# Kernel optimization log

Hardware: AMD Instinct MI355X
Metric: run time of the kernel (lower is better)

## Reference

```python
import jax, jax.numpy as jnp
import numpy as np

D_MODEL = 1024
HIDDEN = 2048
D_STATE = 16
KERN = 3
BATCH = 2
SEQ = 2048


def _layernorm(x, g, b, eps=1e-5):
    m = jnp.mean(x, axis=-1, keepdims=True)
    v = jnp.var(x, axis=-1, keepdims=True)
    return (x - m) * jax.lax.rsqrt(v + eps) * g + b


def setup_inputs() -> dict:
    key = jax.random.key(0)
    ks = jax.random.split(key, 10)
    w_scale = 0.02  # keep pre-activations in a sane range (mimics trained-net init)
    return {
        "x": jax.random.normal(ks[0], (BATCH, SEQ, D_MODEL), jnp.float32),
        "W_x": jax.random.normal(ks[1], (HIDDEN, D_MODEL), jnp.float32) * w_scale,
        "b_x": jnp.zeros((HIDDEN,), jnp.float32),
        "W_g": jax.random.normal(ks[2], (HIDDEN, D_MODEL), jnp.float32) * w_scale,
        "b_g": jnp.zeros((HIDDEN,), jnp.float32),
        "conv_w": jax.random.normal(ks[3], (HIDDEN, 1, KERN), jnp.float32) * 0.3,
        "conv_b": jnp.zeros((HIDDEN,), jnp.float32),
        "A_raw": jax.random.normal(ks[4], (HIDDEN, D_STATE), jnp.float32),
        "B_ssm": jax.random.normal(ks[5], (HIDDEN, D_STATE), jnp.float32),
        "C_ssm": jax.random.normal(ks[6], (HIDDEN, D_STATE), jnp.float32),
        "W_dt": jax.random.normal(ks[7], (HIDDEN, D_MODEL), jnp.float32) * w_scale,
        "b_dt": jnp.zeros((HIDDEN,), jnp.float32),
        "W_out": jax.random.normal(ks[8], (D_MODEL, HIDDEN), jnp.float32) * w_scale,
        "b_out": jnp.zeros((D_MODEL,), jnp.float32),
        "ln_g": jnp.ones((D_MODEL,), jnp.float32),
        "ln_b": jnp.zeros((D_MODEL,), jnp.float32),
    }


def reference(x, W_x, b_x, W_g, b_g, conv_w, conv_b, A_raw, B_ssm, C_ssm,
              W_dt, b_dt, W_out, b_out, ln_g, ln_b):
    # projections: u, gate
    u = jnp.einsum('bld,hd->blh', x, W_x) + b_x                    # [B,L,H]
    g = jax.nn.sigmoid(jnp.einsum('bld,hd->blh', x, W_g) + b_g)    # [B,L,H]
    # depthwise conv over time (padding = kernel//2, 'same' for odd kernel)
    pad = conv_w.shape[-1] // 2
    h = jax.lax.conv_general_dilated(
        jnp.transpose(u, (0, 2, 1)), conv_w,
        window_strides=(1,), padding=[(pad, pad)],
        feature_group_count=conv_w.shape[0],
        dimension_numbers=('NCH', 'OIH', 'NCH')) + conv_b[None, :, None]
    h = jnp.transpose(h, (0, 2, 1))                                # [B,L,H]
    u = u * g + h * (1.0 - g)
    # time-invariant dt per channel (mean over batch & time, clamped)
    dt = jax.nn.softplus(jnp.einsum('bld,hd->blh', x, W_dt) + b_dt).mean(axis=(0, 1))
    dt = jnp.clip(dt, 1e-3, 2.0)                                   # [H]
    # discretize
    A = -jax.nn.softplus(A_raw)                                    # [H,S]
    A_d = jnp.exp(A * dt[:, None])                                 # [H,S]
    B_d = (A_d - 1.0) / (A + 1e-6) * B_ssm                         # [H,S]
    # selective scan: state s[b,h,k] = A_d*s + B_d*u_t ; y = <s, C>
    Bsz, L, H = u.shape
    S = A_d.shape[1]

    def step(carry, u_t):                                          # u_t: [B,H]
        new = A_d[None] * carry + B_d[None] * u_t[:, :, None]      # [B,H,S]
        y_t = jnp.einsum('bhs,hs->bh', new, C_ssm)
        return new, y_t

    init = jnp.zeros((Bsz, H, S), dtype=u.dtype)
    _, ys = jax.lax.scan(step, init, jnp.transpose(u, (1, 0, 2)))  # ys: [L,B,H]
    y = jnp.transpose(ys, (1, 0, 2))                               # [B,L,H]
    out = jnp.einsum('blh,dh->bld', y, W_out) + b_out
    return _layernorm(x + out, ln_g, ln_b)
```

## Files before the change

### kernel.cpp

```cpp
#include <hip/hip_runtime.h>
#include <math.h>

#define D_MODEL 1024
#define HIDDEN  2048
#define D_STATE 16
#define BATCH   2
#define SEQ     2048
#define NTOK    (BATCH*SEQ)
#define CHUNK   32
#define NCHUNK  (SEQ/CHUNK)

typedef __attribute__((ext_vector_type(8))) short bf16x8;
typedef __attribute__((ext_vector_type(8))) unsigned short ushort8;
typedef __attribute__((ext_vector_type(4))) float f32x4;

#define GLOAD_LDS16(gptr, lptr) \
    __builtin_amdgcn_global_load_lds((const __attribute__((address_space(1))) void*)(gptr), \
                                     (__attribute__((address_space(3))) void*)(lptr), 16, 0, 0)

__device__ __forceinline__ float softplus_f(float x) {
    return fmaxf(x, 0.0f) + log1pf(expf(-fabsf(x)));
}
__device__ __forceinline__ float sigmoid_f(float x) {
    return 1.0f / (1.0f + expf(-x));
}
__device__ __forceinline__ ushort f2bf(float f) {
    unsigned u = __float_as_uint(f);
    unsigned r = (u + 0x7fffu + ((u >> 16) & 1u)) >> 16;
    return (ushort)r;
}
__device__ __forceinline__ float bf2f(ushort u) {
    return __uint_as_float(((unsigned)u) << 16);
}

__global__ __launch_bounds__(256) void cvt_all(
    const float* __restrict__ x, const float* __restrict__ Wx,
    const float* __restrict__ Wg, const float* __restrict__ Wdt,
    const float* __restrict__ Wout, ushort* __restrict__ arena)
{
    int i = blockIdx.x * 256 + threadIdx.x;
    const float* src; int base;
    if      (i < 1048576) { src = x;    base = 0; }
    else if (i < 1572864) { src = Wx;   base = 1048576; }
    else if (i < 2097152) { src = Wg;   base = 1572864; }
    else if (i < 2621440) { src = Wdt;  base = 2097152; }
    else                  { src = Wout; base = 2621440; }
    float4 v = reinterpret_cast<const float4*>(src)[i - base];
    ushort4 o = { f2bf(v.x), f2bf(v.y), f2bf(v.z), f2bf(v.w) };
    reinterpret_cast<ushort4*>(arena)[i] = o;
}

__global__ __launch_bounds__(256) void proj_gemm_fused(
    const ushort* __restrict__ xbf, const ushort* __restrict__ Wcat,
    const float* __restrict__ b_x, const float* __restrict__ b_g,
    const float* __restrict__ b_dt, ushort* __restrict__ u_out,
    ushort* __restrict__ g_out, float* __restrict__ dt_sum)
{
    __shared__ ushort S[16384];
    ushort* As = S;
    ushort* Bs = S + 4096;
    const int tid = threadIdx.x, lane = tid & 63, w = tid >> 6;
    const int wm = w & 1, wn = w >> 1;
    const int m0 = blockIdx.x * 128, n0 = blockIdx.y * 128;
    const int quad = lane >> 4, fr = lane & 15;
    const int lr   = lane >> 2;
    const int qsrc = (lane & 3) ^ ((lane >> 3) & 3);
    const int chq  = quad ^ ((fr >> 1) & 3);
    const int K = D_MODEL;

    const size_t ga0 = (size_t)(m0 + w * 16 + lr) * K + qsrc * 8;
    const size_t ga1 = ga0 + (size_t)64 * K;
    const size_t gb0 = (size_t)(n0 + w * 16 + lr) * K + qsrc * 8;
    const size_t gb1 = gb0 + (size_t)64 * K;

    f32x4 acc[4][4];
    #pragma unroll
    for (int i = 0; i < 4; i++)
        #pragma unroll
        for (int j = 0; j < 4; j++)
            acc[i][j] = (f32x4){0.f, 0.f, 0.f, 0.f};

    for (int t = 0; t < K / 32; t++) {
        const size_t koff = (size_t)t * 32;
        GLOAD_LDS16(xbf  + ga0 + koff, &As[w * 512]);
        GLOAD_LDS16(xbf  + ga1 + koff, &As[2048 + w * 512]);
        GLOAD_LDS16(Wcat + gb0 + koff, &Bs[w * 512]);
        GLOAD_LDS16(Wcat + gb1 + koff, &Bs[2048 + w * 512]);
        asm volatile("s_waitcnt vmcnt(0) lgkmcnt(0)" ::: "memory");
        asm volatile("s_barrier" ::: "memory");

        bf16x8 af[4], bfv[4];
        #pragma unroll
        for (int q = 0; q < 4; q++) {
            af[q]  = *reinterpret_cast<const bf16x8*>(&As[(wm * 64 + q * 16 + fr) * 32 + chq * 8]);
            bfv[q] = *reinterpret_cast<const bf16x8*>(&Bs[(wn * 64 + q * 16 + fr) * 32 + chq * 8]);
        }
        #pragma unroll
        for (int ii = 0; ii < 4; ii++)
            #pragma unroll
            for (int jj = 0; jj < 4; jj++)
                acc[ii][jj] = __builtin_amdgcn_mfma_f32_16x16x32_bf16(af[ii], bfv[jj], acc[ii][jj], 0, 0, 0);
        asm volatile("s_barrier" ::: "memory");
    }

    const int region = n0 >> 11;
    const int ncb = n0 & 2047;

    if (region == 2) {
        #pragma unroll
        for (int j = 0; j < 4; j++) {
            int n = ncb + wn * 64 + j * 16 + fr;
            float bj = b_dt[n];
            float s = 0.f;
            #pragma unroll
            for (int i = 0; i < 4; i++)
                #pragma unroll
                for (int r = 0; r < 4; r++)
                    s += softplus_f(acc[i][j][r] + bj);
            s += __shfl_xor(s, 16);
            s += __shfl_xor(s, 32);
            if (lane < 16) atomicAdd(&dt_sum[n], s);
        }
    } else {
        const float* bias = region ? b_g : b_x;
        ushort* out = region ? g_out : u_out;
        ushort* Cs = S;
        __syncthreads();
        #pragma unroll
        for (int j = 0; j < 4; j++) {
            int col = wn * 64 + j * 16 + fr;
            float bj = bias[ncb + col];
            #pragma unroll
            for (int i = 0; i < 4; i++) {
                int row = wm * 64 + i * 16 + quad * 4;
                #pragma unroll
                for (int r = 0; r < 4; r++) {
                    float v = acc[i][j][r] + bj;
                    if (region) v = sigmoid_f(v);
                    Cs[(row + r) * 128 + col] = f2bf(v);
                }
            }
        }
        __syncthreads();
        #pragma unroll
        for (int k = 0; k < 8; k++) {
            int v = k * 256 + tid;
            int row = v >> 4, c = (v & 15) * 8;
            *reinterpret_cast<ushort8*>(&out[(size_t)(m0 + row) * HIDDEN + ncb + c]) =
                *reinterpret_cast<const ushort8*>(&Cs[v * 8]);
        }
    }
}

__global__ __launch_bounds__(256) void gemm_out64(
    const ushort* __restrict__ ybf, const ushort* __restrict__ Wout,
    const float* __restrict__ b_out, const float* __restrict__ x,
    float* __restrict__ resid)
{
    __shared__ ushort S[36864];
    ushort* As = S;
    ushort* Bs = S + 12288;
    const int tid = threadIdx.x, lane = tid & 63, w = tid >> 6;
    const int m0 = blockIdx.x * 64, n0 = blockIdx.y * 128;
    const int quad = lane >> 4, fr = lane & 15;
    const int lr8  = lane >> 3;
    const int q8   = (lane & 7) ^ (lr8 & 7);
    const int K = HIDDEN;

    const size_t ga = (size_t)(m0 + w * 16 + lr8) * K + q8 * 8;
    const size_t gb = (size_t)(n0 + w * 32 + lr8) * K + q8 * 8;

    f32x4 acc[4][2];
    #pragma unroll
    for (int i = 0; i < 4; i++)
        #pragma unroll
        for (int j = 0; j < 2; j++)
            acc[i][j] = (f32x4){0.f, 0.f, 0.f, 0.f};

#define STAGE_OUT(KT, BUF) do {                                                   \
    const size_t ko_ = (size_t)(KT) * 64;                                         \
    GLOAD_LDS16(ybf  + ga + ko_,            &As[(BUF)*4096 + (w*2+0)*512]);       \
    GLOAD_LDS16(ybf  + ga + 8*K + ko_,      &As[(BUF)*4096 + (w*2+1)*512]);       \
    GLOAD_LDS16(Wout + gb + ko_,            &Bs[(BUF)*8192 + (w*4+0)*512]);       \
    GLOAD_LDS16(Wout + gb + 8*K + ko_,      &Bs[(BUF)*8192 + (w*4+1)*512]);       \
    GLOAD_LDS16(Wout + gb + 16*K + ko_,     &Bs[(BUF)*8192 + (w*4+2)*512]);       \
    GLOAD_LDS16(Wout + gb + 24*K + ko_,     &Bs[(BUF)*8192 + (w*4+3)*512]);       \
  } while (0)

    STAGE_OUT(0, 0);
    STAGE_OUT(1, 1);

    int buf = 0;
    for (int t = 0; t < 32; t++) {
        asm volatile("s_waitcnt vmcnt(6) lgkmcnt(0)" ::: "memory");
        asm volatile("s_barrier" ::: "memory");
        int nb = buf + 2; if (nb >= 3) nb -= 3;
        const int kt = (t + 2 < 32) ? (t + 2) : 0;
        STAGE_OUT(kt, nb);

        const ushort* as = &As[buf * 4096];
        const ushort* bs = &Bs[buf * 8192];
        #pragma unroll
        for (int ks = 0; ks < 2; ks++) {
            const int ch = ((ks * 4 + quad) ^ (fr & 7)) * 8;
            bf16x8 af[4], bfv[2];
            #pragma unroll
            for (int mi = 0; mi < 4; mi++)
                af[mi] = *reinterpret_cast<const bf16x8*>(&as[(mi * 16 + fr) * 64 + ch]);
            #pragma unroll
            for (int nj = 0; nj < 2; nj++)
                bfv[nj] = *reinterpret_cast<const bf16x8*>(&bs[(w * 32 + nj * 16 + fr) * 64 + ch]);
            #pragma unroll
            for (int mi = 0; mi < 4; mi++)
                #pragma unroll
                for (int nj = 0; nj < 2; nj++)
                    acc[mi][nj] = __builtin_amdgcn_mfma_f32_16x16x32_bf16(af[mi], bfv[nj], acc[mi][nj], 0, 0, 0);
        }
        buf = (buf == 2) ? 0 : buf + 1;
    }
    asm volatile("s_waitcnt vmcnt(0) lgkmcnt(0)" ::: "memory");
    asm volatile("s_barrier" ::: "memory");
#undef STAGE_OUT

    float* Sf = (float*)S;
    #pragma unroll
    for (int nj = 0; nj < 2; nj++) {
        int col = w * 32 + nj * 16 + fr;
        float bj = b_out[n0 + col];
        #pragma unroll
        for (int mi = 0; mi < 4; mi++) {
            int row = mi * 16 + quad * 4;
            #pragma unroll
            for (int r = 0; r < 4; r++)
                Sf[(row + r) * 128 + col] = acc[mi][nj][r] + bj;
        }
    }
    __syncthreads();
    #pragma unroll
    for (int k = 0; k < 8; k++) {
        int v = k * 256 + tid;
        int row = v >> 5, c = (v & 31) * 4;
        size_t off = (size_t)(m0 + row) * D_MODEL + n0 + c;
        float4 xa = *reinterpret_cast<const float4*>(&x[off]);
        float4 cv = *reinterpret_cast<const float4*>(&Sf[v * 4]);
        float4 o = { cv.x + xa.x, cv.y + xa.y, cv.z + xa.z, cv.w + xa.w };
        *reinterpret_cast<float4*>(&resid[off]) = o;
    }
}

__global__ __launch_bounds__(256) void dt_finalize(
    const float* __restrict__ dt_sum, const float* __restrict__ A_raw,
    const float* __restrict__ B_ssm, float* __restrict__ A_d,
    float* __restrict__ B_d, float* __restrict__ A_dL)
{
    int i = blockIdx.x * 256 + threadIdx.x;
    if (i >= HIDDEN * D_STATE) return;
    int h = i >> 4;
    float dt = dt_sum[h] * (1.0f / NTOK);
    dt = fminf(fmaxf(dt, 1e-3f), 2.0f);
    float Av = -softplus_f(A_raw[i]);
    float Ad = expf(Av * dt);
    float Bd = (Ad - 1.0f) / (Av + 1e-6f) * B_ssm[i];
    A_d[i] = Ad;
    B_d[i] = Bd;
    A_dL[i] = expf(Av * dt * CHUNK);
}

__global__ __launch_bounds__(256) void scan_pass1(
    const ushort* __restrict__ u_bf, const ushort* __restrict__ g_bf,
    const float* __restrict__ conv_w, const float* __restrict__ conv_b,
    const float* __restrict__ A_d, const float* __restrict__ B_d,
    const float* __restrict__ C_ssm,
    ushort* __restrict__ ypart, float* __restrict__ states)
{
    int idx = blockIdx.x * 256 + threadIdx.x;
    int h  = idx & (HIDDEN - 1);
    int bc = idx >> 11;
    int c  = bc & (NCHUNK - 1);
    int b  = bc / NCHUNK;
    float Ad[D_STATE], Bd[D_STATE], Cv[D_STATE], st[D_STATE];
    const float4* a4 = reinterpret_cast<const float4*>(A_d  + h * D_STATE);
    const float4* b4 = reinterpret_cast<const float4*>(B_d  + h * D_STATE);
    const float4* c4 = reinterpret_cast<const float4*>(C_ssm + h * D_STATE);
    #pragma unroll
    for (int q = 0; q < 4; q++) {
        float4 av = a4[q], bv = b4[q], cv = c4[q];
        Ad[q*4+0]=av.x; Ad[q*4+1]=av.y; Ad[q*4+2]=av.z; Ad[q*4+3]=av.w;
        Bd[q*4+0]=bv.x; Bd[q*4+1]=bv.y; Bd[q*4+2]=bv.z; Bd[q*4+3]=bv.w;
        Cv[q*4+0]=cv.x; Cv[q*4+1]=cv.y; Cv[q*4+2]=cv.z; Cv[q*4+3]=cv.w;
    }
    #pragma unroll
    for (int s = 0; s < D_STATE; s++) st[s] = 0.f;

    float w0 = conv_w[h * 3 + 0], w1 = conv_w[h * 3 + 1];
    float w2 = conv_w[h * 3 + 2], cb = conv_b[h];
    const int tok0 = c * CHUNK;
    const size_t base = ((size_t)b * SEQ + tok0) * HIDDEN + h;
    float u_prev = (tok0 > 0) ? bf2f(u_bf[base - HIDDEN]) : 0.f;
    float u_cur  = bf2f(u_bf[base]);
    for (int l = 0; l < CHUNK; l++) {
        float u_next = (tok0 + l + 1 < SEQ) ? bf2f(u_bf[base + (size_t)(l + 1) * HIDDEN]) : 0.f;
        float gv = bf2f(g_bf[base + (size_t)l * HIDDEN]);
        float conv = u_prev * w0 + u_cur * w1 + u_next * w2 + cb;
        float uv = u_cur * gv + conv * (1.0f - gv);
        float y0 = 0.f, y1 = 0.f, y2 = 0.f, y3 = 0.f;
        #pragma unroll
        for (int s = 0; s < D_STATE; s += 4) {
            st[s+0] = fmaf(Ad[s+0], st[s+0], Bd[s+0] * uv);
            st[s+1] = fmaf(Ad[s+1], st[s+1], Bd[s+1] * uv);
            st[s+2] = fmaf(Ad[s+2], st[s+2], Bd[s+2] * uv);
            st[s+3] = fmaf(Ad[s+3], st[s+3], Bd[s+3] * uv);
            y0 = fmaf(st[s+0], Cv[s+0], y0);
            y1 = fmaf(st[s+1], Cv[s+1], y1);
            y2 = fmaf(st[s+2], Cv[s+2], y2);
            y3 = fmaf(st[s+3], Cv[s+3], y3);
        }
        ypart[base + (size_t)l * HIDDEN] = f2bf((y0 + y1) + (y2 + y3));
        u_prev = u_cur; u_cur = u_next;
    }
    float4* sp = reinterpret_cast<float4*>(states + ((size_t)bc * HIDDEN + h) * D_STATE);
    #pragma unroll
    for (int q = 0; q < 4; q++)
        sp[q] = (float4){st[q*4+0], st[q*4+1], st[q*4+2], st[q*4+3]};
}

__global__ __launch_bounds__(256) void scan_pass2(
    float* __restrict__ states, const float* __restrict__ A_dL)
{
    int idx = blockIdx.x * 256 + threadIdx.x;
    int s = idx & 15;
    int h = (idx >> 4) & (HIDDEN - 1);
    int b = idx >> 15;
    float aL = A_dL[h * D_STATE + s];
    float carry = 0.f;
    const size_t cstride = (size_t)HIDDEN * D_STATE;
    float* p = states + ((size_t)b * NCHUNK * HIDDEN + h) * D_STATE + s;
    #pragma unroll 1
    for (int cb = 0; cb < NCHUNK / 8; cb++) {
        float fin[8];
        #pragma unroll
        for (int j = 0; j < 8; j++) fin[j] = p[(size_t)j * cstride];
        #pragma unroll
        for (int j = 0; j < 8; j++) {
            p[(size_t)j * cstride] = carry;
            carry = fmaf(aL, carry, fin[j]);
        }
        p += 8 * cstride;
    }
}

__global__ __launch_bounds__(256) void scan_pass3(
    const ushort* __restrict__ ypart, const float* __restrict__ states,
    const float* __restrict__ A_d, const float* __restrict__ C_ssm,
    ushort* __restrict__ ybf)
{
    int idx = blockIdx.x * 256 + threadIdx.x;
    int h  = idx & (HIDDEN - 1);
    int bc = idx >> 11;
    int c  = bc & (NCHUNK - 1);
    int b  = bc / NCHUNK;
    float Ad[D_STATE], t[D_STATE];
    const float* sp = states + ((size_t)bc * HIDDEN + h) * D_STATE;
    #pragma unroll
    for (int s = 0; s < D_STATE; s++) {
        float a = A_d[h * D_STATE + s];
        Ad[s] = a;
        t[s] = C_ssm[h * D_STATE + s] * a * sp[s];
    }
    const size_t base = ((size_t)b * SEQ + (size_t)c * CHUNK) * HIDDEN + h;
    for (int l = 0; l < CHUNK; l++) {
        float c0 = 0.f, c1 = 0.f;
        #pragma unroll
        for (int s = 0; s < D_STATE; s += 2) {
            c0 += t[s];
            c1 += t[s + 1];
            t[s] *= Ad[s];
            t[s + 1] *= Ad[s + 1];
        }
        ybf[base + (size_t)l * HIDDEN] = f2bf(bf2f(ypart[base + (size_t)l * HIDDEN]) + (c0 + c1));
    }
}

__global__ __launch_bounds__(256) void ln_kernel(
    const float* __restrict__ resid, const float* __restrict__ ln_g,
    const float* __restrict__ ln_b, float* __restrict__ out)
{
    int row = blockIdx.x;
    int tid = threadIdx.x;
    const float4 v = reinterpret_cast<const float4*>(resid + (size_t)row * D_MODEL)[tid];
    float s  = v.x + v.y + v.z + v.w;
    float ss = v.x * v.x + v.y * v.y + v.z * v.z + v.w * v.w;
    #pragma unroll
    for (int off = 32; off > 0; off >>= 1) {
        s  += __shfl_down(s, off);
        ss += __shfl_down(ss, off);
    }
    __shared__ float sbuf[4], ssbuf[4];
    int wid = tid >> 6, lane = tid & 63;
    if (lane == 0) { sbuf[wid] = s; ssbuf[wid] = ss; }
    __syncthreads();
    float tot  = sbuf[0] + sbuf[1] + sbuf[2] + sbuf[3];
    float tot2 = ssbuf[0] + ssbuf[1] + ssbuf[2] + ssbuf[3];
    float mean = tot * (1.0f / D_MODEL);
    float var  = tot2 * (1.0f / D_MODEL) - mean * mean;
    float rstd = rsqrtf(var + 1e-5f);
    const float4 gv = reinterpret_cast<const float4*>(ln_g)[tid];
    const float4 bv = reinterpret_cast<const float4*>(ln_b)[tid];
    float4 o;
    o.x = (v.x - mean) * rstd * gv.x + bv.x;
    o.y = (v.y - mean) * rstd * gv.y + bv.y;
    o.z = (v.z - mean) * rstd * gv.z + bv.z;
    o.w = (v.w - mean) * rstd * gv.w + bv.w;
    reinterpret_cast<float4*>(out + (size_t)row * D_MODEL)[tid] = o;
}

extern "C" void kernel_launch(void* const* d_in, const int* in_sizes, int n_in,
                              void* d_out, int out_size, void* d_ws, size_t ws_size,
                              hipStream_t stream) {
    const float* x      = (const float*)d_in[0];
    const float* W_x    = (const float*)d_in[1];
    const float* b_x    = (const float*)d_in[2];
    const float* W_g    = (const float*)d_in[3];
    const float* b_g    = (const float*)d_in[4];
    const float* conv_w = (const float*)d_in[5];
    const float* conv_b = (const float*)d_in[6];
    const float* A_raw  = (const float*)d_in[7];
    const float* B_ssm  = (const float*)d_in[8];
    const float* C_ssm  = (const float*)d_in[9];
    const float* W_dt   = (const float*)d_in[10];
    const float* b_dt   = (const float*)d_in[11];
    const float* W_out  = (const float*)d_in[12];
    const float* b_out  = (const float*)d_in[13];
    const float* ln_g   = (const float*)d_in[14];
    const float* ln_b   = (const float*)d_in[15];

    char* W = (char*)d_ws;
    ushort* arena   = (ushort*)(W);
    ushort* x_bf    = arena;
    ushort* Wcat    = arena + 4194304;
    ushort* Wout_bf = arena + 10485760;
    ushort* u_bf    = (ushort*)(W + (24ull << 20));
    ushort* g_bf    = (ushort*)(W + (40ull << 20));
    ushort* ypart   = (ushort*)(W + (56ull << 20));
    float*  resid   = (float*)(W + (40ull << 20));
    float*  states  = (float*)(W);
    float*  dt_sum  = (float*)(W + (80ull << 20));
    float*  A_d     = (float*)(W + (80ull << 20) + 65536);
    float*  B_d     = (float*)(W + (80ull << 20) + 65536 + 131072);
    float*  A_dL    = (float*)(W + (80ull << 20) + 65536 + 262144);
    ushort* y_bf    = u_bf;

    hipMemsetAsync(dt_sum, 0, HIDDEN * sizeof(float), stream);

    dim3 blk(256);
    cvt_all<<<12288, blk, 0, stream>>>(x, W_x, W_g, W_dt, W_out, arena);

    dim3 grid_proj(NTOK / 128, 3 * HIDDEN / 128);
    proj_gemm_fused<<<grid_proj, blk, 0, stream>>>(x_bf, Wcat, b_x, b_g, b_dt,
                                                   u_bf, g_bf, dt_sum);
    dt_finalize<<<(HIDDEN * D_STATE) / 256, blk, 0, stream>>>(dt_sum, A_raw, B_ssm,
                                                              A_d, B_d, A_dL);
    scan_pass1<<<(BATCH * NCHUNK * HIDDEN) / 256, blk, 0, stream>>>(
        u_bf, g_bf, conv_w, conv_b, A_d, B_d, C_ssm, ypart, states);
    scan_pass2<<<(BATCH * HIDDEN * D_STATE) / 256, blk, 0, stream>>>(states, A_dL);
    scan_pass3<<<(BATCH * NCHUNK * HIDDEN) / 256, blk, 0, stream>>>(ypart, states, A_d,
                                                                    C_ssm, y_bf);
    dim3 grid_out(NTOK / 64, D_MODEL / 128);
    gemm_out64<<<grid_out, blk, 0, stream>>>(y_bf, Wout_bf, b_out, x, resid);
    ln_kernel<<<NTOK, blk, 0, stream>>>(resid, ln_g, ln_b, (float*)d_out);
}
```

Measured before the change: 306.3 us.

## Enlarge projection GEMM tile to 256x128 with triple-buffered async LDS pipeline

The projection GEMM moves from a 128x128 tile, where each wave computes 64x64, to a 256x128 tile where each wave computes 64x128 (4x8 MFMA accumulators). The global-to-LDS loads now use a three-buffer ring, prefetching two k-steps ahead and waiting with a partial vmcnt, so memory latency overlaps with MFMA work instead of stalling on every step. The aim is more data reuse per LDS load and better latency hiding. In exchange it uses more registers and LDS per block, and halves the grid along M, which may lower occupancy.

Result: no change. 303.3 us (-1.0%).

```diff
diff --git a/kernel.cpp b/kernel.cpp
--- a/kernel.cpp
+++ b/kernel.cpp
@@ -50,73 +50,88 @@
     reinterpret_cast<ushort4*>(arena)[i] = o;
 }
 
-__global__ __launch_bounds__(256) void proj_gemm_fused(
+__global__ __launch_bounds__(256, 2) void proj_gemm_fused(
     const ushort* __restrict__ xbf, const ushort* __restrict__ Wcat,
     const float* __restrict__ b_x, const float* __restrict__ b_g,
     const float* __restrict__ b_dt, ushort* __restrict__ u_out,
     ushort* __restrict__ g_out, float* __restrict__ dt_sum)
 {
-    __shared__ ushort S[16384];
+    __shared__ ushort S[36864];
     ushort* As = S;
-    ushort* Bs = S + 4096;
+    ushort* Bs = S + 24576;
     const int tid = threadIdx.x, lane = tid & 63, w = tid >> 6;
-    const int wm = w & 1, wn = w >> 1;
-    const int m0 = blockIdx.x * 128, n0 = blockIdx.y * 128;
+    const int m0 = blockIdx.x * 256, n0 = blockIdx.y * 128;
     const int quad = lane >> 4, fr = lane & 15;
     const int lr   = lane >> 2;
     const int qsrc = (lane & 3) ^ ((lane >> 3) & 3);
     const int chq  = quad ^ ((fr >> 1) & 3);
     const int K = D_MODEL;
 
-    const size_t ga0 = (size_t)(m0 + w * 16 + lr) * K + qsrc * 8;
-    const size_t ga1 = ga0 + (size_t)64 * K;
-    const size_t gb0 = (size_t)(n0 + w * 16 + lr) * K + qsrc * 8;
-    const size_t gb1 = gb0 + (size_t)64 * K;
-
-    f32x4 acc[4][4];
+    const size_t gaB = (size_t)(m0 + w * 64 + lr) * K + qsrc * 8;
+    const size_t gbB = (size_t)(n0 + w * 32 + lr) * K + qsrc * 8;
+
+    f32x4 acc[4][8];
     #pragma unroll
     for (int i = 0; i < 4; i++)
         #pragma unroll
-        for (int j = 0; j < 4; j++)
+        for (int j = 0; j < 8; j++)
             acc[i][j] = (f32x4){0.f, 0.f, 0.f, 0.f};
 
-    for (int t = 0; t < K / 32; t++) {
-        const size_t koff = (size_t)t * 32;
-        GLOAD_LDS16(xbf  + ga0 + koff, &As[w * 512]);
-        GLOAD_LDS16(xbf  + ga1 + koff, &As[2048 + w * 512]);
-        GLOAD_LDS16(Wcat + gb0 + koff, &Bs[w * 512]);
-        GLOAD_LDS16(Wcat + gb1 + koff, &Bs[2048 + w * 512]);
-        asm volatile("s_waitcnt vmcnt(0) lgkmcnt(0)" ::: "memory");
+#define STAGE_P(KT, BUF) do {                                                     \
+    const size_t ko_ = (size_t)(KT) * 32;                                         \
+    GLOAD_LDS16(xbf  + gaB + 0 * 16 * K + ko_, &As[(BUF)*8192 + (w*64 +  0)*32]); \
+    GLOAD_LDS16(xbf  + gaB + 1 * 16 * K + ko_, &As[(BUF)*8192 + (w*64 + 16)*32]); \
+    GLOAD_LDS16(xbf  + gaB + 2 * 16 * K + ko_, &As[(BUF)*8192 + (w*64 + 32)*32]); \
+    GLOAD_LDS16(xbf  + gaB + 3 * 16 * K + ko_, &As[(BUF)*8192 + (w*64 + 48)*32]); \
+    GLOAD_LDS16(Wcat + gbB + 0 * 16 * K + ko_, &Bs[(BUF)*4096 + (w*32 +  0)*32]); \
+    GLOAD_LDS16(Wcat + gbB + 1 * 16 * K + ko_, &Bs[(BUF)*4096 + (w*32 + 16)*32]); \
+  } while (0)
+
+    STAGE_P(0, 0);
+    STAGE_P(1, 1);
+
+    int buf = 0;
+    for (int t = 0; t < 32; t++) {
+        asm volatile("s_waitcnt vmcnt(6) lgkmcnt(0)" ::: "memory");
         asm volatile("s_barrier" ::: "memory");
-
-        bf16x8 af[4], bfv[4];
-        #pragma unroll
-        for (int q = 0; q < 4; q++) {
-            af[q]  = *reinterpret_cast<const bf16x8*>(&As[(wm * 64 + q * 16 + fr) * 32 + chq * 8]);
-            bfv[q] = *reinterpret_cast<const bf16x8*>(&Bs[(wn * 64 + q * 16 + fr) * 32 + chq * 8]);
-        }
-        #pragma unroll
-        for (int ii = 0; ii < 4; ii++)
-            #pragma unroll
-            for (int jj = 0; jj < 4; jj++)
-                acc[ii][jj] = __builtin_amdgcn_mfma_f32_16x16x32_bf16(af[ii], bfv[jj], acc[ii][jj], 0, 0, 0);
-        asm volatile("s_barrier" ::: "memory");
-    }
+        int nb = buf + 2; if (nb >= 3) nb -= 3;
+        const int kt = (t + 2 < 32) ? (t + 2) : 0;
+        STAGE_P(kt, nb);
+
+        const ushort* as = &As[buf * 8192];
+        const ushort* bs = &Bs[buf * 4096];
+        bf16x8 af[4], bfv[8];
+        #pragma unroll
+        for (int mi = 0; mi < 4; mi++)
+            af[mi] = *reinterpret_cast<const bf16x8*>(&as[(w * 64 + mi * 16 + fr) * 32 + chq * 8]);
+        #pragma unroll
+        for (int nj = 0; nj < 8; nj++)
+            bfv[nj] = *reinterpret_cast<const bf16x8*>(&bs[(nj * 16 + fr) * 32 + chq * 8]);
+        #pragma unroll
+        for (int mi = 0; mi < 4; mi++)
+            #pragma unroll
+            for (int nj = 0; nj < 8; nj++)
+                acc[mi][nj] = __builtin_amdgcn_mfma_f32_16x16x32_bf16(af[mi], bfv[nj], acc[mi][nj], 0, 0, 0);
+        buf = (buf == 2) ? 0 : buf + 1;
+    }
+    asm volatile("s_waitcnt vmcnt(0) lgkmcnt(0)" ::: "memory");
+    asm volatile("s_barrier" ::: "memory");
+#undef STAGE_P
 
     const int region = n0 >> 11;
     const int ncb = n0 & 2047;
 
     if (region == 2) {
         #pragma unroll
-        for (int j = 0; j < 4; j++) {
-            int n = ncb + wn * 64 + j * 16 + fr;
+        for (int nj = 0; nj < 8; nj++) {
+            int n = ncb + nj * 16 + fr;
             float bj = b_dt[n];
             float s = 0.f;
             #pragma unroll
-            for (int i = 0; i < 4; i++)
+            for (int mi = 0; mi < 4; mi++)
                 #pragma unroll
                 for (int r = 0; r < 4; r++)
-                    s += softplus_f(acc[i][j][r] + bj);
+                    s += softplus_f(acc[mi][nj][r] + bj);
             s += __shfl_xor(s, 16);
             s += __shfl_xor(s, 32);
             if (lane < 16) atomicAdd(&dt_sum[n], s);
@@ -127,15 +142,15 @@
         ushort* Cs = S;
         __syncthreads();
         #pragma unroll
-        for (int j = 0; j < 4; j++) {
-            int col = wn * 64 + j * 16 + fr;
+        for (int nj = 0; nj < 8; nj++) {
+            int col = nj * 16 + fr;
             float bj = bias[ncb + col];
             #pragma unroll
-            for (int i = 0; i < 4; i++) {
-                int row = wm * 64 + i * 16 + quad * 4;
+            for (int mi = 0; mi < 4; mi++) {
+                int row = w * 64 + mi * 16 + quad * 4;
                 #pragma unroll
                 for (int r = 0; r < 4; r++) {
-                    float v = acc[i][j][r] + bj;
+                    float v = acc[mi][nj][r] + bj;
                     if (region) v = sigmoid_f(v);
                     Cs[(row + r) * 128 + col] = f2bf(v);
                 }
@@ -143,7 +158,7 @@
         }
         __syncthreads();
         #pragma unroll
-        for (int k = 0; k < 8; k++) {
+        for (int k = 0; k < 16; k++) {
             int v = k * 256 + tid;
             int row = v >> 4, c = (v & 15) * 8;
             *reinterpret_cast<ushort8*>(&out[(size_t)(m0 + row) * HIDDEN + ncb + c]) =
@@ -455,7 +470,7 @@
     dim3 blk(256);
     cvt_all<<<12288, blk, 0, stream>>>(x, W_x, W_g, W_dt, W_out, arena);
 
-    dim3 grid_proj(NTOK / 128, 3 * HIDDEN / 128);
+    dim3 grid_proj(NTOK / 256, 3 * HIDDEN / 128);
     proj_gemm_fused<<<grid_proj, blk, 0, stream>>>(x_bf, Wcat, b_x, b_g, b_dt,
                                                    u_bf, g_bf, dt_sum);
     dt_finalize<<<(HIDDEN * D_STATE) / 256, blk, 0, stream>>>(dt_sum, A_raw, B_ssm,
```

## Pipeline projection GEMM with triple-buffered A and register-direct B loads

Applied to the files above, without the earlier changes.

Rewrites the projection GEMM main loop so the activation tile is staged into a three-slot LDS ring two steps ahead, while weight fragments are loaded straight from global memory into registers and double-buffered, with partial vmcnt waits in place of full drains. This is meant to hide global-load latency behind the MFMA work that previously sat idle waiting on each tile. Separately, the dt_sum zeroing memset is folded into the conversion kernel to remove one launch. The trade-offs are more registers in use and uncoalesced per-lane weight reads that skip LDS, which may lower occupancy or bandwidth efficiency.

New measurement: 354.1 us. 15.6% more time.

```diff
diff --git a/kernel.cpp b/kernel.cpp
--- a/kernel.cpp
+++ b/kernel.cpp
@@ -36,8 +36,14 @@
 __global__ __launch_bounds__(256) void cvt_all(
     const float* __restrict__ x, const float* __restrict__ Wx,
     const float* __restrict__ Wg, const float* __restrict__ Wdt,
-    const float* __restrict__ Wout, ushort* __restrict__ arena)
-{
+    const float* __restrict__ Wout, ushort* __restrict__ arena,
+    float* __restrict__ dt_sum)
+{
+    if (blockIdx.x == 0) {
+        float4 z = {0.f, 0.f, 0.f, 0.f};
+        reinterpret_cast<float4*>(dt_sum)[threadIdx.x]       = z;
+        reinterpret_cast<float4*>(dt_sum)[256 + threadIdx.x] = z;
+    }
     int i = blockIdx.x * 256 + threadIdx.x;
     const float* src; int base;
     if      (i < 1048576) { src = x;    base = 0; }
@@ -58,7 +64,6 @@
 {
     __shared__ ushort S[16384];
     ushort* As = S;
-    ushort* Bs = S + 4096;
     const int tid = threadIdx.x, lane = tid & 63, w = tid >> 6;
     const int wm = w & 1, wn = w >> 1;
     const int m0 = blockIdx.x * 128, n0 = blockIdx.y * 128;
@@ -68,10 +73,12 @@
     const int chq  = quad ^ ((fr >> 1) & 3);
     const int K = D_MODEL;
 
-    const size_t ga0 = (size_t)(m0 + w * 16 + lr) * K + qsrc * 8;
-    const size_t ga1 = ga0 + (size_t)64 * K;
-    const size_t gb0 = (size_t)(n0 + w * 16 + lr) * K + qsrc * 8;
-    const size_t gb1 = gb0 + (size_t)64 * K;
+    const size_t ga0 = (size_t)(m0 + w * 32 + lr) * K + qsrc * 8;
+    const size_t ga1 = ga0 + (size_t)16 * K;
+    const size_t gb0 = (size_t)(n0 + wn * 64 +  0 + fr) * K + quad * 8;
+    const size_t gb1 = (size_t)(n0 + wn * 64 + 16 + fr) * K + quad * 8;
+    const size_t gb2 = (size_t)(n0 + wn * 64 + 32 + fr) * K + quad * 8;
+    const size_t gb3 = (size_t)(n0 + wn * 64 + 48 + fr) * K + quad * 8;
 
     f32x4 acc[4][4];
     #pragma unroll
@@ -80,28 +87,72 @@
         for (int j = 0; j < 4; j++)
             acc[i][j] = (f32x4){0.f, 0.f, 0.f, 0.f};
 
-    for (int t = 0; t < K / 32; t++) {
-        const size_t koff = (size_t)t * 32;
-        GLOAD_LDS16(xbf  + ga0 + koff, &As[w * 512]);
-        GLOAD_LDS16(xbf  + ga1 + koff, &As[2048 + w * 512]);
-        GLOAD_LDS16(Wcat + gb0 + koff, &Bs[w * 512]);
-        GLOAD_LDS16(Wcat + gb1 + koff, &Bs[2048 + w * 512]);
-        asm volatile("s_waitcnt vmcnt(0) lgkmcnt(0)" ::: "memory");
+#define PJ_LOADB(d0, d1, d2, d3, T) do {                                          \
+    const size_t kb_ = ((T) < 32) ? (size_t)(T) * 32 : 0;                         \
+    d0 = *reinterpret_cast<const bf16x8*>(&Wcat[gb0 + kb_]);                      \
+    d1 = *reinterpret_cast<const bf16x8*>(&Wcat[gb1 + kb_]);                      \
+    d2 = *reinterpret_cast<const bf16x8*>(&Wcat[gb2 + kb_]);                      \
+    d3 = *reinterpret_cast<const bf16x8*>(&Wcat[gb3 + kb_]);                      \
+  } while (0)
+
+#define PJ_STAGEA(T, BUFP) do {                                                   \
+    const size_t ko_ = ((T) < 32) ? (size_t)(T) * 32 : 0;                         \
+    GLOAD_LDS16(xbf + ga0 + ko_, (BUFP) + w * 1024);                              \
+    GLOAD_LDS16(xbf + ga1 + ko_, (BUFP) + w * 1024 + 512);                        \
+  } while (0)
+
+#define PJ_BODY(ABUF, B0, B1, B2, B3) do {                                        \
+    bf16x8 af0 = *reinterpret_cast<const bf16x8*>(&(ABUF)[(wm*64 +  0 + fr)*32 + chq*8]); \
+    bf16x8 af1 = *reinterpret_cast<const bf16x8*>(&(ABUF)[(wm*64 + 16 + fr)*32 + chq*8]); \
+    bf16x8 af2 = *reinterpret_cast<const bf16x8*>(&(ABUF)[(wm*64 + 32 + fr)*32 + chq*8]); \
+    bf16x8 af3 = *reinterpret_cast<const bf16x8*>(&(ABUF)[(wm*64 + 48 + fr)*32 + chq*8]); \
+    acc[0][0]=__builtin_amdgcn_mfma_f32_16x16x32_bf16(af0,B0,acc[0][0],0,0,0);    \
+    acc[0][1]=__builtin_amdgcn_mfma_f32_16x16x32_bf16(af0,B1,acc[0][1],0,0,0);    \
+    acc[0][2]=__builtin_amdgcn_mfma_f32_16x16x32_bf16(af0,B2,acc[0][2],0,0,0);    \
+    acc[0][3]=__builtin_amdgcn_mfma_f32_16x16x32_bf16(af0,B3,acc[0][3],0,0,0);    \
+    acc[1][0]=__builtin_amdgcn_mfma_f32_16x16x32_bf16(af1,B0,acc[1][0],0,0,0);    \
+    acc[1][1]=__builtin_amdgcn_mfma_f32_16x16x32_bf16(af1,B1,acc[1][1],0,0,0);    \
+    acc[1][2]=__builtin_amdgcn_mfma_f32_16x16x32_bf16(af1,B2,acc[1][2],0,0,0);    \
+    acc[1][3]=__builtin_amdgcn_mfma_f32_16x16x32_bf16(af1,B3,acc[1][3],0,0,0);    \
+    acc[2][0]=__builtin_amdgcn_mfma_f32_16x16x32_bf16(af2,B0,acc[2][0],0,0,0);    \
+    acc[2][1]=__builtin_amdgcn_mfma_f32_16x16x32_bf16(af2,B1,acc[2][1],0,0,0);    \
+    acc[2][2]=__builtin_amdgcn_mfma_f32_16x16x32_bf16(af2,B2,acc[2][2],0,0,0);    \
+    acc[2][3]=__builtin_amdgcn_mfma_f32_16x16x32_bf16(af2,B3,acc[2][3],0,0,0);    \
+    acc[3][0]=__builtin_amdgcn_mfma_f32_16x16x32_bf16(af3,B0,acc[3][0],0,0,0);    \
+    acc[3][1]=__builtin_amdgcn_mfma_f32_16x16x32_bf16(af3,B1,acc[3][1],0,0,0);    \
+    acc[3][2]=__builtin_amdgcn_mfma_f32_16x16x32_bf16(af3,B2,acc[3][2],0,0,0);    \
+    acc[3][3]=__builtin_amdgcn_mfma_f32_16x16x32_bf16(af3,B3,acc[3][3],0,0,0);    \
+  } while (0)
+
+    PJ_STAGEA(0, As);
+    PJ_STAGEA(1, As + 4096);
+    bf16x8 bA0, bA1, bA2, bA3, bB0, bB1, bB2, bB3;
+    PJ_LOADB(bA0, bA1, bA2, bA3, 0);
+
+    ushort* Asb0 = As;
+    ushort* Asb1 = As + 4096;
+    ushort* Asb2 = As + 8192;
+    #pragma unroll 1
+    for (int t = 0; t < 32; t += 2) {
+        asm volatile("s_waitcnt vmcnt(6) lgkmcnt(0)" ::: "memory");
         asm volatile("s_barrier" ::: "memory");
-
-        bf16x8 af[4], bfv[4];
-        #pragma unroll
-        for (int q = 0; q < 4; q++) {
-            af[q]  = *reinterpret_cast<const bf16x8*>(&As[(wm * 64 + q * 16 + fr) * 32 + chq * 8]);
-            bfv[q] = *reinterpret_cast<const bf16x8*>(&Bs[(wn * 64 + q * 16 + fr) * 32 + chq * 8]);
-        }
-        #pragma unroll
-        for (int ii = 0; ii < 4; ii++)
-            #pragma unroll
-            for (int jj = 0; jj < 4; jj++)
-                acc[ii][jj] = __builtin_amdgcn_mfma_f32_16x16x32_bf16(af[ii], bfv[jj], acc[ii][jj], 0, 0, 0);
+        PJ_STAGEA(t + 2, Asb2);
+        PJ_LOADB(bB0, bB1, bB2, bB3, t + 1);
+        PJ_BODY(Asb0, bA0, bA1, bA2, bA3);
+
+        asm volatile("s_waitcnt vmcnt(6) lgkmcnt(0)" ::: "memory");
         asm volatile("s_barrier" ::: "memory");
-    }
+        PJ_STAGEA(t + 3, Asb0);
+        PJ_LOADB(bA0, bA1, bA2, bA3, t + 2);
+        PJ_BODY(Asb1, bB0, bB1, bB2, bB3);
+
+        ushort* tmp = Asb0; Asb0 = Asb2; Asb2 = Asb1; Asb1 = tmp;
+    }
+    asm volatile("s_waitcnt vmcnt(0) lgkmcnt(0)" ::: "memory");
+    asm volatile("s_barrier" ::: "memory");
+#undef PJ_BODY
+#undef PJ_STAGEA
+#undef PJ_LOADB
 
     const int region = n0 >> 11;
     const int ncb = n0 & 2047;
@@ -125,7 +176,6 @@
         const float* bias = region ? b_g : b_x;
         ushort* out = region ? g_out : u_out;
         ushort* Cs = S;
-        __syncthreads();
         #pragma unroll
         for (int j = 0; j < 4; j++) {
             int col = wn * 64 + j * 16 + fr;
@@ -450,10 +500,8 @@
     float*  A_dL    = (float*)(W + (80ull << 20) + 65536 + 262144);
     ushort* y_bf    = u_bf;
 
-    hipMemsetAsync(dt_sum, 0, HIDDEN * sizeof(float), stream);
-
     dim3 blk(256);
-    cvt_all<<<12288, blk, 0, stream>>>(x, W_x, W_g, W_dt, W_out, arena);
+    cvt_all<<<12288, blk, 0, stream>>>(x, W_x, W_g, W_dt, W_out, arena, dt_sum);
 
     dim3 grid_proj(NTOK / 128, 3 * HIDDEN / 128);
     proj_gemm_fused<<<grid_proj, blk, 0, stream>>>(x_bf, Wcat, b_x, b_g, b_dt,
```
